# Kernel optimization log

Hardware: AMD Instinct MI355X
Metric: run time of the kernel (lower is better)

The kernel has to match this reference:

```python
import jax, jax.numpy as jnp
import numpy as np

SCALE_DIM = 64  # output_size, used as 1/sqrt(d) scale per source code


def setup_inputs() -> dict:
    key = jax.random.key(0)
    ks = jax.random.split(key, 6)
    B, S, D_IN, D_OUT = 4, 4096, 512, 64
    return {
        "key_inputs": jax.random.normal(ks[0], (B, S, D_IN), dtype=jnp.float32),
        "value_inputs": jax.random.normal(ks[1], (B, S, D_IN), dtype=jnp.float32),
        "query_inputs": jax.random.normal(ks[2], (B, S, D_IN), dtype=jnp.float32),
        "Wq": jax.random.normal(ks[3], (D_IN, D_OUT), dtype=jnp.float32) * 0.05,
        "Wk": jax.random.normal(ks[4], (D_IN, D_OUT), dtype=jnp.float32) * 0.05,
        "Wv": jax.random.normal(ks[5], (D_IN, D_OUT), dtype=jnp.float32) * 0.05,
    }


def reference(key_inputs, value_inputs, query_inputs, Wq, Wk, Wv):
    # QKV projections: [B,S,D_in] x [D_in,D_out] -> [B,S,D_out]
    Q = jnp.einsum("bsd,de->bse", query_inputs, Wq)
    K = jnp.einsum("bsd,de->bse", key_inputs, Wk)
    V = jnp.einsum("bsd,de->bse", value_inputs, Wv)
    d = K.shape[2]
    # scores: [B, Sq, Sk]
    scores = jnp.einsum("bqe,bke->bqk", Q, K) / jnp.sqrt(jnp.float32(d))
    # causal mask: strictly-upper-triangular -inf (source: transpose(tril(-inf, -1)))
    Sq, Sk = Q.shape[1], K.shape[1]
    causal = jnp.tril(jnp.ones((Sq, Sk), dtype=bool))
    scores = jnp.where(causal[None, :, :], scores, -jnp.inf)
    attn = jax.nn.softmax(scores, axis=-1)
    Z = jnp.einsum("bqk,bke->bqe", attn, V)
    return Z
```

## Files before the change

### kernel.cpp

```cpp
#include <hip/hip_runtime.h>
#include <hip/hip_bf16.h>

#define BATCH 4
#define SEQ   4096
#define DIN   512
#define DOUT  64

typedef __attribute__((ext_vector_type(4))) float f32x4;
typedef __attribute__((ext_vector_type(8))) short bf16x8;
typedef __attribute__((ext_vector_type(4))) short bf16x4;

__device__ __forceinline__ f32x4 mfma16(bf16x8 a, bf16x8 b, f32x4 c) {
    return __builtin_amdgcn_mfma_f32_16x16x32_bf16(a, b, c, 0, 0, 0);
}
__device__ __forceinline__ f32x4 mfma16k(bf16x4 a, bf16x4 b, f32x4 c) {
    return __builtin_amdgcn_mfma_f32_16x16x16bf16_1k(a, b, c, 0, 0, 0);
}

__device__ __forceinline__ short f2bf(float f) {
    union { float f; unsigned u; } x; x.f = f;
    unsigned r = x.u + 0x7FFFu + ((x.u >> 16) & 1u);
    return (short)(r >> 16);
}

__device__ __forceinline__ unsigned pack_bf2(float lo, float hi) {
    union { float f; unsigned u; } a, b; a.f = lo; b.f = hi;
    return __builtin_amdgcn_perm(b.u, a.u, 0x07060302u);
}

__device__ __forceinline__ void dma16(const void* g, void* l) {
    __builtin_amdgcn_global_load_lds(
        (const __attribute__((address_space(1))) void*)g,
        (__attribute__((address_space(3))) void*)l, 16, 0, 0);
}

#define QSCALE 0.1803368801111204f

__global__ __launch_bounds__(256) void wconv_kernel(
    const float* __restrict__ Wq, const float* __restrict__ Wk,
    const float* __restrict__ Wv, short* __restrict__ Wt)
{
    const int m = blockIdx.y;
    const float* W = (m == 0) ? Wq : (m == 1) ? Wk : Wv;
    const int idx = blockIdx.x * 256 + threadIdx.x;
    const int k = idx >> 6;
    const int n = idx & 63;
    Wt[m * (DOUT * DIN) + n * DIN + k] = f2bf(W[idx]);
}

__global__ __launch_bounds__(256) void proj_kernel(
    const float* __restrict__ Xq, const float* __restrict__ Xk, const float* __restrict__ Xv,
    const short* __restrict__ Wt,
    short* __restrict__ Qb, short* __restrict__ Kb, short* __restrict__ Vt)
{
    __shared__ __align__(16) char smem[2][24576];

    const int m = blockIdx.y;
    const float* X  = (m == 0) ? Xq : (m == 1) ? Xk : Xv;
    const short* Wm = Wt + m * (DOUT * DIN);

    const int tid  = threadIdx.x;
    const int wv   = tid >> 6;
    const int lane = tid & 63;
    const int quad = lane >> 4;
    const int l16  = lane & 15;
    const long waveRow = (long)blockIdx.x * 64 + wv * 16;

    const float* xg = X  + (waveRow + l16) * DIN + quad * 8;
    const short* wg = Wm + (long)(wv * 16 + l16) * DIN + quad * 8;

    f32x4 acc[4];
    #pragma unroll
    for (int e = 0; e < 4; ++e) acc[e] = (f32x4){0.f, 0.f, 0.f, 0.f};

#define STAGE_PROJ(B) do {                                   \
        char* xb_ = &smem[(B)][0] + wv * 4096;               \
        char* wb_ = &smem[(B)][0] + 16384 + wv * 2048;       \
        dma16(xg,      xb_);                                 \
        dma16(xg + 4,  xb_ + 1024);                          \
        dma16(xg + 32, xb_ + 2048);                          \
        dma16(xg + 36, xb_ + 3072);                          \
        dma16(wg,      wb_);                                 \
        dma16(wg + 32, wb_ + 1024);                          \
    } while (0)

    STAGE_PROJ(0);
    xg += 64; wg += 64;

    #pragma unroll
    for (int kt = 0; kt < 8; ++kt) {
        const int cur = kt & 1;
        if (kt < 7) {
            if (cur) { STAGE_PROJ(0); } else { STAGE_PROJ(1); }
            xg += 64; wg += 64;
            __builtin_amdgcn_sched_barrier(0);
            asm volatile("s_waitcnt vmcnt(6)" ::: "memory");
            __builtin_amdgcn_sched_barrier(0);
        } else {
            __builtin_amdgcn_sched_barrier(0);
            asm volatile("s_waitcnt vmcnt(0)" ::: "memory");
            __builtin_amdgcn_sched_barrier(0);
        }
        __builtin_amdgcn_s_barrier();

        const char* xb = &smem[cur][0] + wv * 4096;
        const char* wb = &smem[cur][0] + 16384;
        #pragma unroll
        for (int c2 = 0; c2 < 2; ++c2) {
            float4 xa = *(const float4*)(xb + c2 * 2048 + lane * 16);
            float4 xc = *(const float4*)(xb + c2 * 2048 + 1024 + lane * 16);
            bf16x8 af;
            af[0] = f2bf(xa.x); af[1] = f2bf(xa.y); af[2] = f2bf(xa.z); af[3] = f2bf(xa.w);
            af[4] = f2bf(xc.x); af[5] = f2bf(xc.y); af[6] = f2bf(xc.z); af[7] = f2bf(xc.w);
            #pragma unroll
            for (int e = 0; e < 4; ++e) {
                bf16x8 bf = *(const bf16x8*)(wb + (e * 2 + c2) * 1024 + lane * 16);
                if (m < 2) acc[e] = mfma16(af, bf, acc[e]);
                else       acc[e] = mfma16(bf, af, acc[e]);
            }
        }
        if (kt < 7) __builtin_amdgcn_s_barrier();
    }
#undef STAGE_PROJ

    if (m < 2) {
        short* O = (m == 0) ? Qb : Kb;
        const float sc = (m == 0) ? QSCALE : 1.0f;
        #pragma unroll
        for (int e = 0; e < 4; ++e)
            #pragma unroll
            for (int r = 0; r < 4; ++r)
                O[(waveRow + quad * 4 + r) * DOUT + e * 16 + l16] = f2bf(acc[e][r] * sc);
    } else {
        const long b = waveRow >> 12;
        const long s = waveRow & (SEQ - 1);
        #pragma unroll
        for (int e = 0; e < 4; ++e)
            #pragma unroll
            for (int r = 0; r < 4; ++r)
                Vt[(b * DOUT + e * 16 + quad * 4 + r) * SEQ + s + l16] = f2bf(acc[e][r]);
    }
}

__global__ __launch_bounds__(512, 4) void flash_kernel(
    const short* __restrict__ Qb, const short* __restrict__ Kb,
    const short* __restrict__ Vt, float* __restrict__ Out)
{
    __shared__ __align__(16) char smem[2][32768];

    const int i    = blockIdx.x;
    const int b    = (i & 7) >> 1;
    const int half = i >> 8;
    const int v    = (((i >> 3) & 31) << 1) | (i & 1);
    const int t    = half ? v : (127 - v);

    const int tid  = threadIdx.x;
    const int wv   = tid >> 6;
    const int lane = tid & 63;
    const int quad = lane >> 4;
    const int l16  = lane & 15;
    const int wq   = wv >> 2;
    const int wk   = wv & 3;
    const int q0w  = t * 32 + wq * 16;

    const short* Qp = Qb + ((long)b * SEQ + q0w + l16) * DOUT + quad * 8;
    bf16x8 qf0 = *(const bf16x8*)(Qp);
    bf16x8 qf1 = *(const bf16x8*)(Qp + 32);

    const short* Kbase  = Kb + (long)b * SEQ * DOUT;
    const short* VbaseG = Vt + (long)b * DOUT * SEQ;

    const short* gk = Kbase + (long)(wv * 16 + l16) * DOUT + quad * 8;
    const int erow = 4 * wv + quad;
    const int cgr  = l16 ^ (erow & 15);
    const short* gv = VbaseG + (long)erow * SEQ + cgr * 8;

    f32x4 acc[4];
    #pragma unroll
    for (int e = 0; e < 4; ++e) acc[e] = (f32x4){0.f, 0.f, 0.f, 0.f};
    float mrow = -1e30f, lrow = 0.f;

    const int q_hi   = q0w + 15;
    const int qg     = q0w + l16;
    const int wfirst = wk * 32;
    const int R      = t / 4 + 1;

#define STAGE_KV(B, KV0) do {                                         \
        char* kb_ = &smem[(B)][0];                                    \
        char* vb_ = &smem[(B)][0] + 16384;                            \
        const short* gkp_ = gk + (long)(KV0) * DOUT;                  \
        dma16(gkp_,      kb_ + (2 * wv) * 1024);                      \
        dma16(gkp_ + 32, kb_ + (2 * wv + 1) * 1024);                  \
        const short* gvp_ = gv + (KV0);                               \
        dma16(gvp_,            vb_ + (wv)     * 1024);                \
        dma16(gvp_ + 32 * SEQ, vb_ + (wv + 8) * 1024);                \
    } while (0)

    STAGE_KV(0, 0);
    __syncthreads();

    for (int r = 0; r < R; ++r) {
        const int kv0 = r * 128;
        const int cur = r & 1;
        if (r + 1 < R) STAGE_KV(cur ^ 1, kv0 + 128);

        if ((kv0 + wfirst) <= q_hi) {
            const char* kb = &smem[cur][0];
            const char* vb = &smem[cur][0] + 16384;

            f32x4 sc[2];
            #pragma unroll
            for (int kh = 0; kh < 2; ++kh) {
                const int slot = (wk * 2 + kh) * 2;
                bf16x8 k0 = *(const bf16x8*)(kb + slot * 1024 + lane * 16);
                bf16x8 k1 = *(const bf16x8*)(kb + (slot + 1) * 1024 + lane * 16);
                f32x4 z = (f32x4){0.f, 0.f, 0.f, 0.f};
                z = mfma16(k0, qf0, z);
                z = mfma16(k1, qf1, z);
                sc[kh] = z;
            }

            if (kv0 + wfirst + 31 > q0w) {
                #pragma unroll
                for (int kh = 0; kh < 2; ++kh)
                    #pragma unroll
                    for (int rr = 0; rr < 4; ++rr)
                        sc[kh][rr] = ((kv0 + wfirst + kh * 16 + quad * 4 + rr) <= qg)
                                   ? sc[kh][rr] : -1e30f;
            }

            float tm = fmaxf(fmaxf(fmaxf(sc[0][0], sc[0][1]), fmaxf(sc[0][2], sc[0][3])),
                             fmaxf(fmaxf(sc[1][0], sc[1][1]), fmaxf(sc[1][2], sc[1][3])));
            tm = fmaxf(tm, __shfl_xor(tm, 16, 64));
            tm = fmaxf(tm, __shfl_xor(tm, 32, 64));
            if (!__all(tm <= mrow)) {
                const float mn = fmaxf(mrow, tm);
                const float alpha = __builtin_amdgcn_exp2f(mrow - mn);
                mrow = mn;
                lrow *= alpha;
                #pragma unroll
                for (int e = 0; e < 4; ++e)
                    #pragma unroll
                    for (int rr = 0; rr < 4; ++rr) acc[e][rr] *= alpha;
            }
            float p[2][4];
            float rs0 = 0.f, rs1 = 0.f;
            #pragma unroll
            for (int kh = 0; kh < 2; ++kh)
                #pragma unroll
                for (int rr = 0; rr < 4; ++rr) {
                    p[kh][rr] = __builtin_amdgcn_exp2f(sc[kh][rr] - mrow);
                    if (kh == 0) rs0 += p[kh][rr]; else rs1 += p[kh][rr];
                }
            float rs = rs0 + rs1;
            rs += __shfl_xor(rs, 16, 64);
            rs += __shfl_xor(rs, 32, 64);
            lrow += rs;

            union { unsigned u[2]; bf16x4 v; } pf[2];
            #pragma unroll
            for (int kh = 0; kh < 2; ++kh) {
                pf[kh].u[0] = pack_bf2(p[kh][0], p[kh][1]);
                pf[kh].u[1] = pack_bf2(p[kh][2], p[kh][3]);
            }

            #pragma unroll
            for (int kh = 0; kh < 2; ++kh) {
                const int gbase = wk * 4 + kh * 2 + (quad >> 1);
                #pragma unroll
                for (int et = 0; et < 4; ++et) {
                    const int e = et * 16 + l16;
                    bf16x4 cv = *(const bf16x4*)(vb + e * 256
                                   + ((gbase ^ (e & 15)) * 16) + (quad & 1) * 8);
                    acc[et] = mfma16k(cv, pf[kh].v, acc[et]);
                }
            }
        }
        __syncthreads();
    }
#undef STAGE_KV

    float* s_m   = (float*)&smem[0][0];
    float* s_l   = s_m + 128;
    float* s_acc = s_l + 128;

    if (quad == 0) { s_m[wv * 16 + l16] = mrow; s_l[wv * 16 + l16] = lrow; }
    #pragma unroll
    for (int et = 0; et < 4; ++et)
        #pragma unroll
        for (int rr = 0; rr < 4; ++rr)
            s_acc[(wv * 16 + l16) * 65 + et * 16 + quad * 4 + rr] = acc[et][rr];
    __syncthreads();

    const int col   = tid & 63;
    const int rbase = (tid >> 6) * 4;
    float* outp = Out + ((long)b * SEQ + t * 32) * DOUT;
    #pragma unroll
    for (int k = 0; k < 4; ++k) {
        const int row = rbase + k;
        const int w0  = (row >> 4) * 4;
        const int lr  = row & 15;
        const float m0 = s_m[(w0 + 0) * 16 + lr];
        const float m1 = s_m[(w0 + 1) * 16 + lr];
        const float m2 = s_m[(w0 + 2) * 16 + lr];
        const float m3 = s_m[(w0 + 3) * 16 + lr];
        const float mM = fmaxf(fmaxf(m0, m1), fmaxf(m2, m3));
        const float a0 = __builtin_amdgcn_exp2f(m0 - mM);
        const float a1 = __builtin_amdgcn_exp2f(m1 - mM);
        const float a2 = __builtin_amdgcn_exp2f(m2 - mM);
        const float a3 = __builtin_amdgcn_exp2f(m3 - mM);
        const float li = a0 * s_l[(w0 + 0) * 16 + lr] + a1 * s_l[(w0 + 1) * 16 + lr]
                       + a2 * s_l[(w0 + 2) * 16 + lr] + a3 * s_l[(w0 + 3) * 16 + lr];
        const float o  = a0 * s_acc[((w0 + 0) * 16 + lr) * 65 + col]
                       + a1 * s_acc[((w0 + 1) * 16 + lr) * 65 + col]
                       + a2 * s_acc[((w0 + 2) * 16 + lr) * 65 + col]
                       + a3 * s_acc[((w0 + 3) * 16 + lr) * 65 + col];
        outp[row * DOUT + col] = o / li;
    }
}

extern "C" void kernel_launch(void* const* d_in, const int* in_sizes, int n_in,
                              void* d_out, int out_size, void* d_ws, size_t ws_size,
                              hipStream_t stream) {
    const float* key_in   = (const float*)d_in[0];
    const float* value_in = (const float*)d_in[1];
    const float* query_in = (const float*)d_in[2];
    const float* Wq = (const float*)d_in[3];
    const float* Wk = (const float*)d_in[4];
    const float* Wv = (const float*)d_in[5];
    float* out = (float*)d_out;

    short* Qb = (short*)d_ws;
    short* Kb = Qb + (long)BATCH * SEQ * DOUT;
    short* Vt = Kb + (long)BATCH * SEQ * DOUT;
    short* Wt = Vt + (long)BATCH * SEQ * DOUT;

    dim3 wgrid((DOUT * DIN) / 256, 3);
    wconv_kernel<<<wgrid, 256, 0, stream>>>(Wq, Wk, Wv, Wt);

    dim3 pgrid(BATCH * SEQ / 64, 3);
    proj_kernel<<<pgrid, 256, 0, stream>>>(query_in, key_in, value_in,
                                           Wt, Qb, Kb, Vt);

    flash_kernel<<<dim3(SEQ / 32 * BATCH), 512, 0, stream>>>(Qb, Kb, Vt, out);
}
```

Measured before the change: 170.2 us.

## Split causal KV range across two blocks per query tile with merge kernel

Each query tile's KV loop is split into two halves processed by separate blocks, doubling the grid from 512 to 1024 blocks. The blocks write unnormalized partial accumulators plus row max and sum to workspace, and a new merge kernel combines them with log-sum-exp rescaling. This targets load imbalance and tail effects from long causal tiles. In exchange it adds a kernel launch, extra global traffic for the partials, and workspace usage. For small t, R>>1 can be zero, which leaves the first half with no work.

```diff
diff --git a/kernel.cpp b/kernel.cpp
--- a/kernel.cpp
+++ b/kernel.cpp
@@ -144,15 +144,16 @@
 
 __global__ __launch_bounds__(512, 4) void flash_kernel(
     const short* __restrict__ Qb, const short* __restrict__ Kb,
-    const short* __restrict__ Vt, float* __restrict__ Out)
+    const short* __restrict__ Vt, float* __restrict__ Pacc,
+    float* __restrict__ Pml)
 {
     __shared__ __align__(16) char smem[2][32768];
 
     const int i    = blockIdx.x;
     const int b    = (i & 7) >> 1;
-    const int half = i >> 8;
-    const int v    = (((i >> 3) & 31) << 1) | (i & 1);
-    const int t    = half ? v : (127 - v);
+    const int j2   = ((i >> 3) << 1) | (i & 1);
+    const int t    = 127 - (j2 >> 1);
+    const int half = j2 & 1;
 
     const int tid  = threadIdx.x;
     const int wv   = tid >> 6;
@@ -184,6 +185,8 @@
     const int qg     = q0w + l16;
     const int wfirst = wk * 32;
     const int R      = t / 4 + 1;
+    const int S      = half ? (R >> 1) : 0;
+    const int E      = half ? R : (R >> 1);
 
 #define STAGE_KV(B, KV0) do {                                         \
         char* kb_ = &smem[(B)][0];                                    \
@@ -196,87 +199,90 @@
         dma16(gvp_ + 32 * SEQ, vb_ + (wv + 8) * 1024);                \
     } while (0)
 
-    STAGE_KV(0, 0);
-    __syncthreads();
-
-    for (int r = 0; r < R; ++r) {
-        const int kv0 = r * 128;
-        const int cur = r & 1;
-        if (r + 1 < R) STAGE_KV(cur ^ 1, kv0 + 128);
-
-        if ((kv0 + wfirst) <= q_hi) {
-            const char* kb = &smem[cur][0];
-            const char* vb = &smem[cur][0] + 16384;
-
-            f32x4 sc[2];
-            #pragma unroll
-            for (int kh = 0; kh < 2; ++kh) {
-                const int slot = (wk * 2 + kh) * 2;
-                bf16x8 k0 = *(const bf16x8*)(kb + slot * 1024 + lane * 16);
-                bf16x8 k1 = *(const bf16x8*)(kb + (slot + 1) * 1024 + lane * 16);
-                f32x4 z = (f32x4){0.f, 0.f, 0.f, 0.f};
-                z = mfma16(k0, qf0, z);
-                z = mfma16(k1, qf1, z);
-                sc[kh] = z;
-            }
-
-            if (kv0 + wfirst + 31 > q0w) {
+    if (S < E) {
+        STAGE_KV(0, S * 128);
+        __syncthreads();
+
+        int rr2 = 0;
+        for (int r = S; r < E; ++r, ++rr2) {
+            const int kv0 = r * 128;
+            const int cur = rr2 & 1;
+            if (r + 1 < E) STAGE_KV(cur ^ 1, kv0 + 128);
+
+            if ((kv0 + wfirst) <= q_hi) {
+                const char* kb = &smem[cur][0];
+                const char* vb = &smem[cur][0] + 16384;
+
+                f32x4 sc[2];
+                #pragma unroll
+                for (int kh = 0; kh < 2; ++kh) {
+                    const int slot = (wk * 2 + kh) * 2;
+                    bf16x8 k0 = *(const bf16x8*)(kb + slot * 1024 + lane * 16);
+                    bf16x8 k1 = *(const bf16x8*)(kb + (slot + 1) * 1024 + lane * 16);
+                    f32x4 z = (f32x4){0.f, 0.f, 0.f, 0.f};
+                    z = mfma16(k0, qf0, z);
+                    z = mfma16(k1, qf1, z);
+                    sc[kh] = z;
+                }
+
+                if (kv0 + wfirst + 31 > q0w) {
+                    #pragma unroll
+                    for (int kh = 0; kh < 2; ++kh)
+                        #pragma unroll
+                        for (int rr = 0; rr < 4; ++rr)
+                            sc[kh][rr] = ((kv0 + wfirst + kh * 16 + quad * 4 + rr) <= qg)
+                                       ? sc[kh][rr] : -1e30f;
+                }
+
+                float tm = fmaxf(fmaxf(fmaxf(sc[0][0], sc[0][1]), fmaxf(sc[0][2], sc[0][3])),
+                                 fmaxf(fmaxf(sc[1][0], sc[1][1]), fmaxf(sc[1][2], sc[1][3])));
+                tm = fmaxf(tm, __shfl_xor(tm, 16, 64));
+                tm = fmaxf(tm, __shfl_xor(tm, 32, 64));
+                if (!__all(tm <= mrow)) {
+                    const float mn = fmaxf(mrow, tm);
+                    const float alpha = __builtin_amdgcn_exp2f(mrow - mn);
+                    mrow = mn;
+                    lrow *= alpha;
+                    #pragma unroll
+                    for (int e = 0; e < 4; ++e)
+                        #pragma unroll
+                        for (int rr = 0; rr < 4; ++rr) acc[e][rr] *= alpha;
+                }
+                float p[2][4];
+                float rs0 = 0.f, rs1 = 0.f;
                 #pragma unroll
                 for (int kh = 0; kh < 2; ++kh)
                     #pragma unroll
-                    for (int rr = 0; rr < 4; ++rr)
-                        sc[kh][rr] = ((kv0 + wfirst + kh * 16 + quad * 4 + rr) <= qg)
-                                   ? sc[kh][rr] : -1e30f;
+                    for (int rr = 0; rr < 4; ++rr) {
+                        p[kh][rr] = __builtin_amdgcn_exp2f(sc[kh][rr] - mrow);
+                        if (kh == 0) rs0 += p[kh][rr]; else rs1 += p[kh][rr];
+                    }
+                float rs = rs0 + rs1;
+                rs += __shfl_xor(rs, 16, 64);
+                rs += __shfl_xor(rs, 32, 64);
+                lrow += rs;
+
+                union { unsigned u[2]; bf16x4 v; } pf[2];
+                #pragma unroll
+                for (int kh = 0; kh < 2; ++kh) {
+                    pf[kh].u[0] = pack_bf2(p[kh][0], p[kh][1]);
+                    pf[kh].u[1] = pack_bf2(p[kh][2], p[kh][3]);
+                }
+
+                #pragma unroll
+                for (int kh = 0; kh < 2; ++kh) {
+                    const int gbase = wk * 4 + kh * 2 + (quad >> 1);
+                    #pragma unroll
+                    for (int et = 0; et < 4; ++et) {
+                        const int e = et * 16 + l16;
+                        bf16x4 cv = *(const bf16x4*)(vb + e * 256
+                                       + ((gbase ^ (e & 15)) * 16) + (quad & 1) * 8);
+                        acc[et] = mfma16k(cv, pf[kh].v, acc[et]);
+                    }
+                }
             }
-
-            float tm = fmaxf(fmaxf(fmaxf(sc[0][0], sc[0][1]), fmaxf(sc[0][2], sc[0][3])),
-                             fmaxf(fmaxf(sc[1][0], sc[1][1]), fmaxf(sc[1][2], sc[1][3])));
-            tm = fmaxf(tm, __shfl_xor(tm, 16, 64));
-            tm = fmaxf(tm, __shfl_xor(tm, 32, 64));
-            if (!__all(tm <= mrow)) {
-                const float mn = fmaxf(mrow, tm);
-                const float alpha = __builtin_amdgcn_exp2f(mrow - mn);
-                mrow = mn;
-                lrow *= alpha;
-                #pragma unroll
-                for (int e = 0; e < 4; ++e)
-                    #pragma unroll
-                    for (int rr = 0; rr < 4; ++rr) acc[e][rr] *= alpha;
-            }
-            float p[2][4];
-            float rs0 = 0.f, rs1 = 0.f;
-            #pragma unroll
-            for (int kh = 0; kh < 2; ++kh)
-                #pragma unroll
-                for (int rr = 0; rr < 4; ++rr) {
-                    p[kh][rr] = __builtin_amdgcn_exp2f(sc[kh][rr] - mrow);
-                    if (kh == 0) rs0 += p[kh][rr]; else rs1 += p[kh][rr];
-                }
-            float rs = rs0 + rs1;
-            rs += __shfl_xor(rs, 16, 64);
-            rs += __shfl_xor(rs, 32, 64);
-            lrow += rs;
-
-            union { unsigned u[2]; bf16x4 v; } pf[2];
-            #pragma unroll
-            for (int kh = 0; kh < 2; ++kh) {
-                pf[kh].u[0] = pack_bf2(p[kh][0], p[kh][1]);
-                pf[kh].u[1] = pack_bf2(p[kh][2], p[kh][3]);
-            }
-
-            #pragma unroll
-            for (int kh = 0; kh < 2; ++kh) {
-                const int gbase = wk * 4 + kh * 2 + (quad >> 1);
-                #pragma unroll
-                for (int et = 0; et < 4; ++et) {
-                    const int e = et * 16 + l16;
-                    bf16x4 cv = *(const bf16x4*)(vb + e * 256
-                                   + ((gbase ^ (e & 15)) * 16) + (quad & 1) * 8);
-                    acc[et] = mfma16k(cv, pf[kh].v, acc[et]);
-                }
-            }
+            __syncthreads();
         }
-        __syncthreads();
     }
 #undef STAGE_KV
 
@@ -294,7 +300,9 @@
 
     const int col   = tid & 63;
     const int rbase = (tid >> 6) * 4;
-    float* outp = Out + ((long)b * SEQ + t * 32) * DOUT;
+    const long pb   = ((long)b * 2 + half) * 128 + t;
+    float* pacc = Pacc + pb * (32 * 64);
+    float* pml  = Pml  + pb * 32 * 2;
     #pragma unroll
     for (int k = 0; k < 4; ++k) {
         const int row = rbase + k;
@@ -315,8 +323,31 @@
                        + a1 * s_acc[((w0 + 1) * 16 + lr) * 65 + col]
                        + a2 * s_acc[((w0 + 2) * 16 + lr) * 65 + col]
                        + a3 * s_acc[((w0 + 3) * 16 + lr) * 65 + col];
-        outp[row * DOUT + col] = o / li;
+        pacc[row * 64 + col] = o;
+        if (col == 0) { pml[row * 2] = mM; pml[row * 2 + 1] = li; }
     }
+}
+
+__global__ __launch_bounds__(256) void fmerge_kernel(
+    const float* __restrict__ Pacc, const float* __restrict__ Pml,
+    float* __restrict__ Out)
+{
+    const int idx = blockIdx.x * 256 + threadIdx.x;
+    const int col = idx & 63;
+    const int rid = idx >> 6;
+    const int b   = rid >> 12;
+    const int s   = rid & (SEQ - 1);
+    const int t   = s >> 5;
+    const int row = s & 31;
+    const long i0 = (((long)b * 2 + 0) * 128 + t) * 32 + row;
+    const long i1 = (((long)b * 2 + 1) * 128 + t) * 32 + row;
+    const float m0 = Pml[i0 * 2], l0 = Pml[i0 * 2 + 1];
+    const float m1 = Pml[i1 * 2], l1 = Pml[i1 * 2 + 1];
+    const float M  = fmaxf(m0, m1);
+    const float a0 = __builtin_amdgcn_exp2f(m0 - M);
+    const float a1 = __builtin_amdgcn_exp2f(m1 - M);
+    const float o  = a0 * Pacc[i0 * 64 + col] + a1 * Pacc[i1 * 64 + col];
+    Out[idx] = o / (a0 * l0 + a1 * l1);
 }
 
 extern "C" void kernel_launch(void* const* d_in, const int* in_sizes, int n_in,
@@ -334,6 +365,8 @@
     short* Kb = Qb + (long)BATCH * SEQ * DOUT;
     short* Vt = Kb + (long)BATCH * SEQ * DOUT;
     short* Wt = Vt + (long)BATCH * SEQ * DOUT;
+    float* Pacc = (float*)(Wt + 3 * DOUT * DIN);
+    float* Pml  = Pacc + (long)BATCH * 2 * 128 * 32 * 64;
 
     dim3 wgrid((DOUT * DIN) / 256, 3);
     wconv_kernel<<<wgrid, 256, 0, stream>>>(Wq, Wk, Wv, Wt);
@@ -342,5 +375,7 @@
     proj_kernel<<<pgrid, 256, 0, stream>>>(query_in, key_in, value_in,
                                            Wt, Qb, Kb, Vt);
 
-    flash_kernel<<<dim3(SEQ / 32 * BATCH), 512, 0, stream>>>(Qb, Kb, Vt, out);
-}
+    flash_kernel<<<dim3(SEQ / 32 * BATCH * 2), 512, 0, stream>>>(Qb, Kb, Vt, Pacc, Pml);
+
+    fmerge_kernel<<<dim3(BATCH * SEQ * DOUT / 256), 256, 0, stream>>>(Pacc, Pml, out);
+}
```

Measured after the change: 171.3 us. Within noise of the previous version (+0.7%).
